# Kernel optimization log

Measured on AMD Instinct MI355X. Metric: run time of the kernel, lower is better.

Reference implementation:

```python
import jax, jax.numpy as jnp
import numpy as np

KERNEL_MUL = 2.0
KERNEL_NUM = 5


def _mmd(source, target):
    n_s = source.shape[0]
    total = jnp.concatenate([source, target], axis=0)  # (2N, D)
    n = total.shape[0]
    # pairwise squared L2 via a^2 + b^2 - 2ab (avoids (2N,2N,D) intermediate)
    sq = jnp.sum(total * total, axis=1)  # (2N,)
    L2 = sq[:, None] + sq[None, :] - 2.0 * (total @ total.T)  # (2N, 2N)
    # torch uses L2_distance.data for bandwidth -> stop_gradient
    bandwidth = jax.lax.stop_gradient(jnp.sum(L2)) / (n * n - n)
    bandwidth = bandwidth / (KERNEL_MUL ** (KERNEL_NUM // 2))
    # multi-bandwidth RBF sum
    kernels = jnp.zeros_like(L2)
    for i in range(KERNEL_NUM):
        kernels = kernels + jnp.exp(-L2 / (bandwidth * KERNEL_MUL ** i))
    XX = kernels[:n_s, :n_s]
    YY = kernels[n_s:, n_s:]
    XY = kernels[:n_s, n_s:]
    YX = kernels[n_s:, :n_s]
    return jnp.mean(XX) + jnp.mean(YY) - jnp.mean(XY) - jnp.mean(YX)


def setup_inputs() -> dict:
    key = jax.random.key(0)
    k1, k2 = jax.random.split(key)
    source = jax.random.normal(k1, (4096, 256), dtype=jnp.float32)
    target = jax.random.normal(k2, (4096, 256), dtype=jnp.float32) + 0.5
    return {"source": source, "target": target}


def reference(source, target):
    return _mmd(source, target)
```

## Files before the change

kernel.cpp:

```cpp
#include <hip/hip_runtime.h>

typedef short bf16x8 __attribute__((ext_vector_type(8)));
typedef float f32x4 __attribute__((ext_vector_type(4)));

#define KDIM 256
#define BT 128
#define BK 64

__device__ __forceinline__ unsigned short f2bf(float f) {
  unsigned u = __float_as_uint(f);
  unsigned r = (u + 0x7fffu + ((u >> 16) & 1u)) >> 16;
  return (unsigned short)r;
}
__device__ __forceinline__ float bf2f(unsigned short b) {
  return __uint_as_float(((unsigned)b) << 16);
}

__device__ __forceinline__ void async_cp16(const void* g, void* l) {
  __builtin_amdgcn_global_load_lds(
      (const __attribute__((address_space(1))) unsigned int*)g,
      (__attribute__((address_space(3))) unsigned int*)l, 16, 0, 0);
}

__global__ __launch_bounds__(256) void mmd_stage(
    const float* __restrict__ src, const float* __restrict__ tgt, int ns,
    unsigned short* __restrict__ Tbf, float* __restrict__ sq,
    float* __restrict__ scol, float* __restrict__ sum_sq) {
  __shared__ float sp[256];
  __shared__ float rw[4];
  int t = threadIdx.x;
  int lane = t & 63, wave = t >> 6;
  sp[t] = 0.f;
  __syncthreads();
  int sub = t & 31;
  int rsel = t >> 5;
  float colacc[8];
#pragma unroll
  for (int j = 0; j < 8; ++j) colacc[j] = 0.f;
  float tsq = 0.f;
  for (int it = 0; it < 16; ++it) {
    int r = blockIdx.x * 128 + it * 8 + rsel;
    const float* rp = (r < ns) ? (src + (size_t)r * KDIM)
                               : (tgt + (size_t)(r - ns) * KDIM);
    float4 v0 = *(const float4*)(rp + sub * 8);
    float4 v1 = *(const float4*)(rp + sub * 8 + 4);
    float vals[8] = {v0.x, v0.y, v0.z, v0.w, v1.x, v1.y, v1.z, v1.w};
    unsigned pk[4];
    float ssp = 0.f;
#pragma unroll
    for (int j = 0; j < 4; ++j) {
      unsigned short b0 = f2bf(vals[2 * j]);
      unsigned short b1 = f2bf(vals[2 * j + 1]);
      float x0 = bf2f(b0), x1 = bf2f(b1);
      pk[j] = (unsigned)b0 | ((unsigned)b1 << 16);
      ssp += x0 * x0 + x1 * x1;
      colacc[2 * j] += x0;
      colacc[2 * j + 1] += x1;
    }
    *(uint4*)(Tbf + (size_t)r * KDIM + sub * 8) =
        make_uint4(pk[0], pk[1], pk[2], pk[3]);
    tsq += ssp;
    float ss = ssp;
#pragma unroll
    for (int off = 16; off; off >>= 1) ss += __shfl_down(ss, off, 32);
    if (sub == 0) sq[r] = ss;
  }
#pragma unroll
  for (int j = 0; j < 8; ++j) atomicAdd(&sp[sub * 8 + j], colacc[j]);
#pragma unroll
  for (int off = 32; off; off >>= 1) tsq += __shfl_down(tsq, off, 64);
  if (lane == 0) rw[wave] = tsq;
  __syncthreads();
  atomicAdd(&scol[t], sp[t]);
  if (t == 0) atomicAdd(sum_sq, rw[0] + rw[1] + rw[2] + rw[3]);
}

__global__ void mmd_prep2(const float* __restrict__ scol,
                          const float* __restrict__ sum_sq,
                          float* __restrict__ coef, float* __restrict__ accum,
                          int n) {
  int t = threadIdx.x;
  float4 v = *(const float4*)(scol + t * 4);
  float p = v.x * v.x + v.y * v.y + v.z * v.z + v.w * v.w;
#pragma unroll
  for (int off = 32; off; off >>= 1) p += __shfl_down(p, off, 64);
  if (t == 0) {
    double ssq = (double)p;
    double S = (double)sum_sq[0];
    double nn = (double)n;
    double sumL2 = 2.0 * nn * S - 2.0 * ssq;
    double bw = sumL2 / (nn * nn - nn) / 4.0;
#pragma unroll
    for (int i = 0; i < 5; ++i) coef[i] = (float)(-1.0 / (bw * (double)(1 << i)));
    accum[0] = 0.f;
  }
}

__global__ __launch_bounds__(256) void mmd_main(
    const unsigned short* __restrict__ Tbf, const float* __restrict__ sq,
    const float* __restrict__ coef, float* __restrict__ accum, int halfTiles) {
  __shared__ short As[BT * BK];
  __shared__ short Bs[BT * BK];
  __shared__ float sqa[BT];
  __shared__ float sqb[BT];
  __shared__ float red[4];

  int id = blockIdx.x;
  int bi = (int)((sqrtf(8.f * (float)id + 1.f) - 1.f) * 0.5f);
  while ((bi + 1) * (bi + 2) / 2 <= id) ++bi;
  while (bi * (bi + 1) / 2 > id) --bi;
  int bj = id - bi * (bi + 1) / 2;
  int rowBase = bi * BT, colBase = bj * BT;

  int t = threadIdx.x;
  int lane = t & 63, wave = t >> 6;

  if (t < 128) sqa[t] = sq[rowBase + t];
  else sqb[t - 128] = sq[colBase + (t - 128)];

  f32x4 acc[4][4];
#pragma unroll
  for (int a = 0; a < 4; ++a)
#pragma unroll
    for (int b = 0; b < 4; ++b) {
      f32x4 z = {0.f, 0.f, 0.f, 0.f};
      acc[a][b] = z;
    }

  int wrow = (wave >> 1) * 64, wcol = (wave & 1) * 64;
  int lrow = lane >> 3;
  int kgsw = (lane & 7) ^ lrow;
  int frow = lane & 15;
  int kq = lane >> 4;

  for (int c = 0; c < 4; ++c) {
    int k0 = c * BK;
#pragma unroll
    for (int j = 0; j < 4; ++j) {
      int R0 = j * 32 + wave * 8;
      int ldsoff = (j * 256 + wave * 64) * 8;
      async_cp16(Tbf + (size_t)(rowBase + R0 + lrow) * KDIM + k0 + kgsw * 8,
                 &As[ldsoff]);
      async_cp16(Tbf + (size_t)(colBase + R0 + lrow) * KDIM + k0 + kgsw * 8,
                 &Bs[ldsoff]);
    }
    __syncthreads();
#pragma unroll
    for (int ks = 0; ks < 2; ++ks) {
      bf16x8 af[4], bfv[4];
#pragma unroll
      for (int mt = 0; mt < 4; ++mt) {
        int r = wrow + mt * 16 + frow;
        int pg = (ks * 4 + kq) ^ (r & 7);
        af[mt] = *(const bf16x8*)&As[r * BK + pg * 8];
      }
#pragma unroll
      for (int nt = 0; nt < 4; ++nt) {
        int r = wcol + nt * 16 + frow;
        int pg = (ks * 4 + kq) ^ (r & 7);
        bfv[nt] = *(const bf16x8*)&Bs[r * BK + pg * 8];
      }
#pragma unroll
      for (int mt = 0; mt < 4; ++mt)
#pragma unroll
        for (int nt = 0; nt < 4; ++nt)
          acc[mt][nt] = __builtin_amdgcn_mfma_f32_16x16x32_bf16(
              af[mt], bfv[nt], acc[mt][nt], 0, 0, 0);
    }
    __syncthreads();
  }

  float c4 = coef[4];
  float lsum = 0.f;
  int ccol = lane & 15;
  int rb = (lane >> 4) * 4;
#pragma unroll
  for (int mt = 0; mt < 4; ++mt) {
#pragma unroll
    for (int nt = 0; nt < 4; ++nt) {
      float sb = sqb[wcol + nt * 16 + ccol];
#pragma unroll
      for (int rg = 0; rg < 4; ++rg) {
        float g = acc[mt][nt][rg];
        float l2 = sqa[wrow + mt * 16 + rb + rg] + sb - 2.f * g;
        float e = __expf(l2 * c4);
        float v = e;
        e = e * e; v += e;
        e = e * e; v += e;
        e = e * e; v += e;
        e = e * e; v += e;
        lsum += v;
      }
    }
  }
#pragma unroll
  for (int off = 32; off; off >>= 1) lsum += __shfl_down(lsum, off, 64);
  if (lane == 0) red[wave] = lsum;
  __syncthreads();
  if (t == 0) {
    float w = ((bi < halfTiles) == (bj < halfTiles)) ? 1.f : -1.f;
    float f = (bi == bj) ? 1.f : 2.f;
    atomicAdd(accum, w * f * (red[0] + red[1] + red[2] + red[3]));
  }
}

__global__ void mmd_fin(const float* __restrict__ accum, float* __restrict__ out,
                        float inv) {
  out[0] = accum[0] * inv;
}

extern "C" void kernel_launch(void* const* d_in, const int* in_sizes, int n_in,
                              void* d_out, int out_size, void* d_ws,
                              size_t ws_size, hipStream_t stream) {
  const float* src = (const float*)d_in[0];
  const float* tgt = (const float*)d_in[1];
  int ns = in_sizes[0] / KDIM;
  int ntr = in_sizes[1] / KDIM;
  int n = ns + ntr;

  char* ws = (char*)d_ws;
  unsigned short* Tbf = (unsigned short*)ws;
  size_t off = (size_t)n * KDIM * sizeof(unsigned short);
  float* sq = (float*)(ws + off);     off += (size_t)n * 4;
  float* scol = (float*)(ws + off);   off += (size_t)KDIM * 4;
  float* sum_sq = (float*)(ws + off); off += 4;
  float* accum = (float*)(ws + off);  off += 4;
  float* coef = (float*)(ws + off);

  hipMemsetAsync(scol, 0, (KDIM + 2) * sizeof(float), stream);

  mmd_stage<<<n / 128, 256, 0, stream>>>(src, tgt, ns, Tbf, sq, scol, sum_sq);
  mmd_prep2<<<1, 64, 0, stream>>>(scol, sum_sq, coef, accum, n);
  int nb = n / BT;
  int nblk = nb * (nb + 1) / 2;
  mmd_main<<<nblk, 256, 0, stream>>>(Tbf, sq, coef, accum, ns / BT);
  mmd_fin<<<1, 1, 0, stream>>>(accum, (float*)d_out,
                               1.f / ((float)ns * (float)ns));
}
```

Baseline: 118.0 us.

## Fold finalize into main kernel, widen staging grid, streamline exp epilogue

Removes the final single-thread kernel by scaling each block's contribution by 1/ns^2 before the atomic add into the output. prep2 now zeroes the output directly. The staging kernel processes 32 rows per block instead of 128, which gives four times as many blocks to spread the memory-bound conversion across CUs, at the cost of more atomics on the column sums. The epilogue folds log2(e) into the coefficients so it can use exp2 directly, pre-scales the squared norms, and pairs the arithmetic into float2 operations to cut per-element VALU work.

```diff
diff --git a/kernel.cpp b/kernel.cpp
--- a/kernel.cpp
+++ b/kernel.cpp
@@ -38,8 +38,9 @@
 #pragma unroll
   for (int j = 0; j < 8; ++j) colacc[j] = 0.f;
   float tsq = 0.f;
-  for (int it = 0; it < 16; ++it) {
-    int r = blockIdx.x * 128 + it * 8 + rsel;
+#pragma unroll
+  for (int it = 0; it < 4; ++it) {
+    int r = blockIdx.x * 32 + it * 8 + rsel;
     const float* rp = (r < ns) ? (src + (size_t)r * KDIM)
                                : (tgt + (size_t)(r - ns) * KDIM);
     float4 v0 = *(const float4*)(rp + sub * 8);
@@ -77,7 +78,7 @@
 
 __global__ void mmd_prep2(const float* __restrict__ scol,
                           const float* __restrict__ sum_sq,
-                          float* __restrict__ coef, float* __restrict__ accum,
+                          float* __restrict__ coef, float* __restrict__ out,
                           int n) {
   int t = threadIdx.x;
   float4 v = *(const float4*)(scol + t * 4);
@@ -90,15 +91,29 @@
     double nn = (double)n;
     double sumL2 = 2.0 * nn * S - 2.0 * ssq;
     double bw = sumL2 / (nn * nn - nn) / 4.0;
-#pragma unroll
-    for (int i = 0; i < 5; ++i) coef[i] = (float)(-1.0 / (bw * (double)(1 << i)));
-    accum[0] = 0.f;
-  }
+    double l2e = 1.4426950408889634;
+#pragma unroll
+    for (int i = 0; i < 5; ++i)
+      coef[i] = (float)(-l2e / (bw * (double)(1 << i)));
+    out[0] = 0.f;
+  }
+}
+
+__device__ __forceinline__ float2 pk_add(float2 a, float2 b) {
+  return make_float2(a.x + b.x, a.y + b.y);
+}
+__device__ __forceinline__ float2 pk_mul(float2 a, float2 b) {
+  return make_float2(a.x * b.x, a.y * b.y);
+}
+__device__ __forceinline__ float2 pk_fma(float2 a, float2 b, float2 c) {
+  return make_float2(__builtin_fmaf(a.x, b.x, c.x),
+                     __builtin_fmaf(a.y, b.y, c.y));
 }
 
 __global__ __launch_bounds__(256) void mmd_main(
     const unsigned short* __restrict__ Tbf, const float* __restrict__ sq,
-    const float* __restrict__ coef, float* __restrict__ accum, int halfTiles) {
+    const float* __restrict__ coef, float* __restrict__ out, int halfTiles,
+    float inv) {
   __shared__ short As[BT * BK];
   __shared__ short Bs[BT * BK];
   __shared__ float sqa[BT];
@@ -171,28 +186,45 @@
   }
 
   float c4 = coef[4];
-  float lsum = 0.f;
+  float m2c4 = -2.f * c4;
+  float2 m2v = make_float2(m2c4, m2c4);
   int ccol = lane & 15;
   int rb = (lane >> 4) * 4;
+  float ra[16];
+#pragma unroll
+  for (int mt = 0; mt < 4; ++mt)
+#pragma unroll
+    for (int rg = 0; rg < 4; ++rg)
+      ra[mt * 4 + rg] = sqa[wrow + mt * 16 + rb + rg] * c4;
+  float cbv[4];
+#pragma unroll
+  for (int nt = 0; nt < 4; ++nt) cbv[nt] = sqb[wcol + nt * 16 + ccol] * c4;
+
+  float2 lsum2 = make_float2(0.f, 0.f);
 #pragma unroll
   for (int mt = 0; mt < 4; ++mt) {
 #pragma unroll
     for (int nt = 0; nt < 4; ++nt) {
-      float sb = sqb[wcol + nt * 16 + ccol];
-#pragma unroll
-      for (int rg = 0; rg < 4; ++rg) {
-        float g = acc[mt][nt][rg];
-        float l2 = sqa[wrow + mt * 16 + rb + rg] + sb - 2.f * g;
-        float e = __expf(l2 * c4);
-        float v = e;
-        e = e * e; v += e;
-        e = e * e; v += e;
-        e = e * e; v += e;
-        e = e * e; v += e;
-        lsum += v;
+      float cb = cbv[nt];
+#pragma unroll
+      for (int rp = 0; rp < 4; rp += 2) {
+        float2 g = make_float2(acc[mt][nt][rp], acc[mt][nt][rp + 1]);
+        float2 sab = make_float2(ra[mt * 4 + rp] + cb, ra[mt * 4 + rp + 1] + cb);
+        float2 u = pk_fma(g, m2v, sab);
+        float2 e = make_float2(__builtin_amdgcn_exp2f(u.x),
+                               __builtin_amdgcn_exp2f(u.y));
+        float2 e2 = pk_mul(e, e);
+        float2 e4 = pk_mul(e2, e2);
+        float2 e8 = pk_mul(e4, e4);
+        float2 s = pk_add(e, e2);
+        s = pk_add(s, e4);
+        s = pk_add(s, e8);
+        s = pk_fma(e8, e8, s);
+        lsum2 = pk_add(lsum2, s);
       }
     }
   }
+  float lsum = lsum2.x + lsum2.y;
 #pragma unroll
   for (int off = 32; off; off >>= 1) lsum += __shfl_down(lsum, off, 64);
   if (lane == 0) red[wave] = lsum;
@@ -200,13 +232,8 @@
   if (t == 0) {
     float w = ((bi < halfTiles) == (bj < halfTiles)) ? 1.f : -1.f;
     float f = (bi == bj) ? 1.f : 2.f;
-    atomicAdd(accum, w * f * (red[0] + red[1] + red[2] + red[3]));
-  }
-}
-
-__global__ void mmd_fin(const float* __restrict__ accum, float* __restrict__ out,
-                        float inv) {
-  out[0] = accum[0] * inv;
+    atomicAdd(out, w * f * inv * (red[0] + red[1] + red[2] + red[3]));
+  }
 }
 
 extern "C" void kernel_launch(void* const* d_in, const int* in_sizes, int n_in,
@@ -224,16 +251,14 @@
   float* sq = (float*)(ws + off);     off += (size_t)n * 4;
   float* scol = (float*)(ws + off);   off += (size_t)KDIM * 4;
   float* sum_sq = (float*)(ws + off); off += 4;
-  float* accum = (float*)(ws + off);  off += 4;
   float* coef = (float*)(ws + off);
 
-  hipMemsetAsync(scol, 0, (KDIM + 2) * sizeof(float), stream);
-
-  mmd_stage<<<n / 128, 256, 0, stream>>>(src, tgt, ns, Tbf, sq, scol, sum_sq);
-  mmd_prep2<<<1, 64, 0, stream>>>(scol, sum_sq, coef, accum, n);
+  hipMemsetAsync(scol, 0, (KDIM + 1) * sizeof(float), stream);
+
+  mmd_stage<<<n / 32, 256, 0, stream>>>(src, tgt, ns, Tbf, sq, scol, sum_sq);
+  mmd_prep2<<<1, 64, 0, stream>>>(scol, sum_sq, coef, (float*)d_out, n);
   int nb = n / BT;
   int nblk = nb * (nb + 1) / 2;
-  mmd_main<<<nblk, 256, 0, stream>>>(Tbf, sq, coef, accum, ns / BT);
-  mmd_fin<<<1, 1, 0, stream>>>(accum, (float*)d_out,
-                               1.f / ((float)ns * (float)ns));
-}
+  mmd_main<<<nblk, 256, 0, stream>>>(Tbf, sq, coef, (float*)d_out, ns / BT,
+                                     1.f / ((float)ns * (float)ns));
+}
```

Result: faster. 110.9 us (-6.0%).
